# Performance work log

Hardware: AMD Instinct MI355X
Metric: run time of the kernel (lower is better)

Reference implementation:

```python
import jax, jax.numpy as jnp
import numpy as np
import math

B, C, D, NH, L, DFF = 128, 112, 512, 8, 13, 1920
DK = D // NH  # 64
_pos = np.arange(64)
_ranks, _files = _pos // 8, _pos % 8
RIDX = np.clip(_ranks[:, None] - _ranks[None, :], -7, 7) + 7  # [64,64] rel-rank bucket
FIDX = np.clip(_files[:, None] - _files[None, :], -7, 7) + 7  # [64,64] rel-file bucket
DIAG = _ranks + _files        # [64] in [0,14]
ADIAG = _ranks - _files + 7   # [64] in [0,14]


def _ln(x, g, b):
    m = jnp.mean(x, -1, keepdims=True)
    v = jnp.mean((x - m) ** 2, -1, keepdims=True)
    return (x - m) * jax.lax.rsqrt(v + 1e-5) * g + b


def setup_inputs() -> dict:
    key = jax.random.key(0)
    ks = iter(jax.random.split(key, 40))
    nrm = lambda *s: jax.random.normal(next(ks), s, jnp.float32) * 0.02
    return dict(
        x=jax.random.normal(next(ks), (B, C, 8, 8), jnp.float32),
        conv_w=nrm(C, D), conv_b=jnp.zeros(D),
        cls_token=nrm(1, 1, D),
        abs_pos=nrm(1, 64, D),
        file_emb=nrm(8, D), rank_emb=nrm(8, D),
        diag_emb=nrm(15, D), anti_diag_emb=nrm(15, D),
        ln1_g=jnp.ones((L, D)), ln1_b=jnp.zeros((L, D)),
        wq=nrm(L, D, D), bq=jnp.zeros((L, D)),
        wk=nrm(L, D, D), bk=jnp.zeros((L, D)),
        wv=nrm(L, D, D), bv=jnp.zeros((L, D)),
        wo=nrm(L, D, D), bo=jnp.zeros((L, D)),
        rel_bias=nrm(L, 15, 15, NH),
        ln2_g=jnp.ones((L, D)), ln2_b=jnp.zeros((L, D)),
        w_ff1=nrm(L, D, 2 * DFF), b_ff1=jnp.zeros((L, 2 * DFF)),
        w_ff2=nrm(L, DFF, D), b_ff2=jnp.zeros((L, D)),
        out_g=jnp.ones(D), out_b=jnp.zeros(D),
        vw1=nrm(D, D // 2), vb1=jnp.zeros(D // 2),
        vw2=nrm(D // 2, 128), vb2=jnp.zeros(128),
        vw3=nrm(128, 3), vb3=jnp.zeros(3),
        pw=nrm(D, 72), pb=jnp.zeros(72),
    )


def reference(x, conv_w, conv_b, cls_token, abs_pos, file_emb, rank_emb, diag_emb, anti_diag_emb,
              ln1_g, ln1_b, wq, bq, wk, bk, wv, bv, wo, bo, rel_bias, ln2_g, ln2_b,
              w_ff1, b_ff1, w_ff2, b_ff2, out_g, out_b,
              vw1, vb1, vw2, vb2, vw3, vb3, pw, pb):
    Bc = x.shape[0]
    # 1x1 conv == channel-wise linear; flatten spatial (row-major: s = rank*8 + file)
    tok = jnp.einsum('bcs,cd->bsd', x.reshape(Bc, C, 64), conv_w) + conv_b  # [B,64,D]
    pos = abs_pos + file_emb[_files] + rank_emb[_ranks] + diag_emb[DIAG] + anti_diag_emb[ADIAG]
    tok = tok + pos
    h = jnp.concatenate([jnp.broadcast_to(cls_token, (Bc, 1, D)), tok], axis=1)  # [B,65,D]
    scale = 1.0 / math.sqrt(DK)

    def block(hx, p):
        g1, b1, Wq, Bq, Wk, Bk, Wv, Bv, Wo, Bo, rb, g2, b2, W1, B1, W2, B2 = p
        n = _ln(hx, g1, b1)
        q = (n @ Wq + Bq).reshape(Bc, 65, NH, DK).transpose(0, 2, 1, 3)
        k = (n @ Wk + Bk).reshape(Bc, 65, NH, DK).transpose(0, 2, 1, 3)
        v = (n @ Wv + Bv).reshape(Bc, 65, NH, DK).transpose(0, 2, 1, 3)
        # gather relative-position bias [64,64,H] -> [H,65,65] with zero row/col for CLS
        bias = jnp.pad(jnp.transpose(rb[RIDX, FIDX], (2, 0, 1)), ((0, 0), (1, 0), (1, 0)))
        scores = jnp.einsum('bhqd,bhkd->bhqk', q, k) * scale + bias[None]
        a = jax.nn.softmax(scores, axis=-1)
        ctx = jnp.einsum('bhqk,bhkd->bhqd', a, v).transpose(0, 2, 1, 3).reshape(Bc, 65, D)
        hx = hx + ctx @ Wo + Bo
        n2 = _ln(hx, g2, b2)
        u = n2 @ W1 + B1
        u1, u2 = jnp.split(u, 2, axis=-1)
        hx = hx + (jax.nn.gelu(u1, approximate=False) * u2) @ W2 + B2
        return hx, None

    params = (ln1_g, ln1_b, wq, bq, wk, bk, wv, bv, wo, bo, rel_bias,
              ln2_g, ln2_b, w_ff1, b_ff1, w_ff2, b_ff2)
    h, _ = jax.lax.scan(block, h, params)
    h = _ln(h, out_g, out_b)
    cls = h[:, 0]
    v1 = jax.nn.gelu(cls @ vw1 + vb1, approximate=False)
    v2 = jax.nn.gelu(v1 @ vw2 + vb2, approximate=False)
    value = v2 @ vw3 + vb3                 # WDL logits [B,3]
    policy = (h[:, 1:] @ pw + pb).reshape(Bc, -1)  # [B, 64*72]
    return policy, value
```

## Files before the change

kernel.cpp:

```cpp
#include <hip/hip_runtime.h>
#include <stdint.h>

#define NLAYER 13
#define DMODEL 512
#define SEQ    65
#define BATCH  128
#define MROWS  (BATCH*SEQ)
#define NHEAD  8
#define DFFH   1920
#define MTILES 65
#define MBAND  9

typedef __bf16 bf16x8 __attribute__((ext_vector_type(8)));
typedef float  f32x4  __attribute__((ext_vector_type(4)));

__device__ __forceinline__ float bf2f(unsigned short u) {
    union { unsigned int i; float f; } c; c.i = ((unsigned int)u) << 16; return c.f;
}
__device__ __forceinline__ unsigned short f2bf(float f) {
    union { float f; unsigned int i; } c; c.f = f;
    unsigned int u = c.i;
    u += 0x7fffu + ((u >> 16) & 1u);
    return (unsigned short)(u >> 16);
}
__device__ __forceinline__ float gelu_exact(float x) {
    return 0.5f * x * (1.0f + erff(x * 0.70710678118654752f));
}

__global__ __launch_bounds__(256) void transpose_f32_bf16(
    const float* __restrict__ src, unsigned short* __restrict__ dst,
    int R, int C, int Cpad, long srcLS, long dstLS, int rowOff)
{
    __shared__ float tile[32][33];
    int l  = blockIdx.z;
    int c0 = blockIdx.x * 32, r0 = blockIdx.y * 32;
    const float* s = src + (long)l * srcLS;
    unsigned short* d = dst + (long)l * dstLS;
    int tx = threadIdx.x, ty = threadIdx.y;
#pragma unroll
    for (int k = 0; k < 4; k++) {
        int r = r0 + ty + 8*k, c = c0 + tx;
        float v = (r < R && c < C) ? s[(long)r * C + c] : 0.0f;
        tile[ty + 8*k][tx] = v;
    }
    __syncthreads();
#pragma unroll
    for (int k = 0; k < 4; k++) {
        int c = c0 + ty + 8*k, r = r0 + tx;
        if (c < Cpad && r < R)
            d[(long)(rowOff + c) * R + r] = f2bf(tile[tx][ty + 8*k]);
    }
}

__global__ __launch_bounds__(256) void stack_bias_kernel(
    const float* __restrict__ bq, const float* __restrict__ bk,
    const float* __restrict__ bv, float* __restrict__ bqkv)
{
    int idx = blockIdx.x * 256 + threadIdx.x;
    if (idx >= NLAYER * 1536) return;
    int l = idx / 1536, r = idx - l * 1536;
    float v;
    if (r < 512)       v = bq[l*512 + r];
    else if (r < 1024) v = bk[l*512 + r - 512];
    else               v = bv[l*512 + r - 1024];
    bqkv[idx] = v;
}

__global__ __launch_bounds__(256) void embed_kernel(
    const float* __restrict__ x, const float* __restrict__ conv_w,
    const float* __restrict__ conv_b, const float* __restrict__ cls_tok,
    const float* __restrict__ abs_pos, const float* __restrict__ file_emb,
    const float* __restrict__ rank_emb, const float* __restrict__ diag_emb,
    const float* __restrict__ adiag_emb, float* __restrict__ h)
{
    int b = blockIdx.y, sg = blockIdx.x, t = threadIdx.x;
    if (sg == 8) {
        for (int d = t; d < 512; d += 256)
            h[(long)b * SEQ * 512 + d] = cls_tok[d];
        return;
    }
    __shared__ float xs[112][8];
    for (int idx = t; idx < 112*8; idx += 256) {
        int c = idx >> 3, j = idx & 7;
        xs[c][j] = x[((long)b*112 + c)*64 + sg*8 + j];
    }
    __syncthreads();
    int d0 = t, d1 = t + 256;
    float acc0[8] = {}, acc1[8] = {};
    for (int c = 0; c < 112; c++) {
        float w0 = conv_w[c*512 + d0], w1 = conv_w[c*512 + d1];
#pragma unroll
        for (int j = 0; j < 8; j++) { acc0[j] += xs[c][j]*w0; acc1[j] += xs[c][j]*w1; }
    }
#pragma unroll
    for (int j = 0; j < 8; j++) {
        int sq = sg*8 + j, r = sq >> 3, f = sq & 7;
        long row = ((long)b * SEQ + 1 + sq) * 512;
        h[row + d0] = acc0[j] + conv_b[d0] + abs_pos[sq*512+d0] + file_emb[f*512+d0]
                    + rank_emb[r*512+d0] + diag_emb[(r+f)*512+d0] + adiag_emb[(r-f+7)*512+d0];
        h[row + d1] = acc1[j] + conv_b[d1] + abs_pos[sq*512+d1] + file_emb[f*512+d1]
                    + rank_emb[r*512+d1] + diag_emb[(r+f)*512+d1] + adiag_emb[(r-f+7)*512+d1];
    }
}

__global__ __launch_bounds__(256) void ln_kernel(
    const float* __restrict__ hx, const float* __restrict__ g,
    const float* __restrict__ bb, unsigned short* __restrict__ o)
{
    int row  = blockIdx.x * 4 + (threadIdx.x >> 6);
    int lane = threadIdx.x & 63;
    const float4* xr = (const float4*)(hx + (long)row * 512);
    float4 v0 = xr[lane], v1 = xr[lane + 64];
    float s  = v0.x+v0.y+v0.z+v0.w + v1.x+v1.y+v1.z+v1.w;
    float s2 = v0.x*v0.x+v0.y*v0.y+v0.z*v0.z+v0.w*v0.w
             + v1.x*v1.x+v1.y*v1.y+v1.z*v1.z+v1.w*v1.w;
    for (int off = 32; off; off >>= 1) { s += __shfl_xor(s, off); s2 += __shfl_xor(s2, off); }
    float mean = s * (1.0f/512.0f);
    float var  = s2 * (1.0f/512.0f) - mean*mean;
    float rs   = rsqrtf(var + 1e-5f);
    const float4* gr = (const float4*)g; const float4* br = (const float4*)bb;
    float4 g0 = gr[lane], g1 = gr[lane+64], b0 = br[lane], b1 = br[lane+64];
    ushort4 o0, o1;
    o0.x = f2bf((v0.x-mean)*rs*g0.x + b0.x);
    o0.y = f2bf((v0.y-mean)*rs*g0.y + b0.y);
    o0.z = f2bf((v0.z-mean)*rs*g0.z + b0.z);
    o0.w = f2bf((v0.w-mean)*rs*g0.w + b0.w);
    o1.x = f2bf((v1.x-mean)*rs*g1.x + b1.x);
    o1.y = f2bf((v1.y-mean)*rs*g1.y + b1.y);
    o1.z = f2bf((v1.z-mean)*rs*g1.z + b1.z);
    o1.w = f2bf((v1.w-mean)*rs*g1.w + b1.w);
    ushort4* orow = (ushort4*)(o + (long)row * 512);
    orow[lane] = o0; orow[lane + 64] = o1;
}

template<int MODE>
__global__ __launch_bounds__(256) void gemm128(
    const unsigned short* __restrict__ A, const unsigned short* __restrict__ Bt,
    const float* __restrict__ bias, const float* __restrict__ res,
    void* __restrict__ out, int K, int ldo, int nT)
{
    __shared__ __attribute__((aligned(16))) unsigned short As[2*128*32];
    __shared__ __attribute__((aligned(16))) unsigned short Bs[2*128*32];
    int id = blockIdx.x;
    int xcd = id & 7, jj = id >> 3;
    int bn  = jj % nT;
    int mt  = xcd * MBAND + jj / nT;
    if (mt >= MTILES) return;
    int m0 = mt * 128;
    int tid = threadIdx.x;
    int lane = tid & 63, w = tid >> 6;
    int quad = lane >> 4, col = lane & 15;

    int srow = tid >> 2;
    int sc8  = (tid & 3) * 8;

    int br0, br1;
    if (MODE == 2) {
        br0 = bn*64 + srow;
        br1 = 1920 + bn*64 + srow;
    } else {
        br0 = bn*128 + srow;
        br1 = bn*128 + srow + 64;
    }
    const unsigned short* Arow0 = A + (long)(m0 + srow) * K + sc8;
    const unsigned short* Arow1 = A + (long)(m0 + srow + 64) * K + sc8;
    const unsigned short* Brow0 = Bt + (long)br0 * K + sc8;
    const unsigned short* Brow1 = Bt + (long)br1 * K + sc8;

    f32x4 acc[2][8] = {};

    int4 ca0 = *(const int4*)(Arow0);
    int4 ca1 = *(const int4*)(Arow1);
    int4 cb0 = *(const int4*)(Brow0);
    int4 cb1 = *(const int4*)(Brow1);
    *(int4*)(&As[srow*32 + sc8])        = ca0;
    *(int4*)(&As[(srow+64)*32 + sc8])   = ca1;
    *(int4*)(&Bs[srow*32 + sc8])        = cb0;
    *(int4*)(&Bs[(srow+64)*32 + sc8])   = cb1;
    ca0 = *(const int4*)(Arow0 + 32);
    ca1 = *(const int4*)(Arow1 + 32);
    cb0 = *(const int4*)(Brow0 + 32);
    cb1 = *(const int4*)(Brow1 + 32);
    __syncthreads();

#define GSTEP(BUFC, BUFN, kt)                                                  \
    {                                                                          \
        bf16x8 af[2], bfr[8];                                                  \
        _Pragma("unroll")                                                      \
        for (int i = 0; i < 2; i++)                                            \
            af[i] = *(const bf16x8*)(&As[(BUFC) + (w*32 + i*16 + col)*32 + quad*8]); \
        _Pragma("unroll")                                                      \
        for (int t = 0; t < 8; t++)                                            \
            bfr[t] = *(const bf16x8*)(&Bs[(BUFC) + (t*16 + col)*32 + quad*8]); \
        if ((kt) + 32 < K) {                                                   \
            *(int4*)(&As[(BUFN) + srow*32 + sc8])      = ca0;                  \
            *(int4*)(&As[(BUFN) + (srow+64)*32 + sc8]) = ca1;                  \
            *(int4*)(&Bs[(BUFN) + srow*32 + sc8])      = cb0;                  \
            *(int4*)(&Bs[(BUFN) + (srow+64)*32 + sc8]) = cb1;                  \
            if ((kt) + 64 < K) {                                               \
                ca0 = *(const int4*)(Arow0 + (kt) + 64);                       \
                ca1 = *(const int4*)(Arow1 + (kt) + 64);                       \
                cb0 = *(const int4*)(Brow0 + (kt) + 64);                       \
                cb1 = *(const int4*)(Brow1 + (kt) + 64);                       \
            }                                                                  \
        }                                                                      \
        _Pragma("unroll")                                                      \
        for (int i = 0; i < 2; i++)                                            \
        _Pragma("unroll")                                                      \
            for (int t = 0; t < 8; t++)                                        \
                acc[i][t] = __builtin_amdgcn_mfma_f32_16x16x32_bf16(af[i], bfr[t], acc[i][t], 0, 0, 0); \
        __syncthreads();                                                       \
    }

    for (int k0 = 0; k0 < K; k0 += 64) {
        GSTEP(0,    4096, k0);
        GSTEP(4096, 0,    k0 + 32);
    }
#undef GSTEP

    if (MODE == 2) {
        unsigned short* O = (unsigned short*)out;
        int gn0 = bn * 64;
#pragma unroll
        for (int i = 0; i < 2; i++)
#pragma unroll
        for (int t = 0; t < 4; t++) {
            int c = t*16 + col;
            float b1v = bias[gn0 + c];
            float b2v = bias[1920 + gn0 + c];
#pragma unroll
            for (int r = 0; r < 4; r++) {
                int m = m0 + w*32 + i*16 + quad*4 + r;
                float u1 = acc[i][t][r]   + b1v;
                float u2 = acc[i][t+4][r] + b2v;
                O[(long)m * DFFH + gn0 + c] = f2bf(gelu_exact(u1) * u2);
            }
        }
        return;
    }
    int n0 = bn * 128;
#pragma unroll
    for (int i = 0; i < 2; i++)
#pragma unroll
    for (int t = 0; t < 8; t++) {
        int cg = n0 + t*16 + col;
        float bv = (MODE == 3) ? (cg < 72 ? bias[cg] : 0.0f) : bias[cg];
#pragma unroll
        for (int r = 0; r < 4; r++) {
            int m = m0 + w*32 + i*16 + quad*4 + r;
            float v = acc[i][t][r] + bv;
            if (MODE == 0) {
                ((unsigned short*)out)[(long)m * ldo + cg] = f2bf(v);
            } else if (MODE == 1) {
                ((float*)out)[(long)m * ldo + cg] = res[(long)m * ldo + cg] + v;
            } else {
                if (cg < 72) {
                    int b2 = m / 65, s = m - b2 * 65;
                    if (s > 0)
                        ((float*)out)[(long)b2 * 4608 + (s - 1) * 72 + cg] = v;
                }
            }
        }
    }
}

__global__ __launch_bounds__(256) void attn_mfma_kernel(
    const unsigned short* __restrict__ qkv,
    const float* __restrict__ rel_bias,
    unsigned short* __restrict__ ctx,
    int layer)
{
    constexpr int QS = 72;
    constexpr int VS = 104;
    constexpr int SS = 68;
    constexpr int PS = 104;
    __shared__ __attribute__((aligned(16))) unsigned short Qs[80*QS];
    __shared__ __attribute__((aligned(16))) unsigned short Ks[80*QS];
    __shared__ __attribute__((aligned(16))) unsigned short Vt[64*VS];
    __shared__ __attribute__((aligned(16))) float Sf[65*SS];
    __shared__ __attribute__((aligned(16))) unsigned short Pb[80*PS];
    __shared__ float bias_s[225];

    int h = blockIdx.x, b = blockIdx.y, t = threadIdx.x;
    int lane = t & 63, w = t >> 6;
    int quad = lane >> 4, col = lane & 15;

    for (int i = t; i < 225; i += 256)
        bias_s[i] = rel_bias[((long)layer*225 + i)*8 + h];

    for (int i = t; i < 65*8; i += 256) {
        int s = i >> 3, c8 = (i & 7) * 8;
        const unsigned short* row = qkv + ((long)(b*65+s))*1536 + h*64 + c8;
        int4 qv = *(const int4*)(row);
        int4 kv = *(const int4*)(row + 512);
        int4 vv = *(const int4*)(row + 1024);
        unsigned short qsc[8];
        const unsigned short* qp = (const unsigned short*)&qv;
#pragma unroll
        for (int j = 0; j < 8; j++) qsc[j] = f2bf(bf2f(qp[j]) * 0.125f);
        *(int4*)&Qs[s*QS + c8] = *(const int4*)qsc;
        *(int4*)&Ks[s*QS + c8] = kv;
        const unsigned short* vp = (const unsigned short*)&vv;
#pragma unroll
        for (int j = 0; j < 8; j++) Vt[(c8+j)*VS + s] = vp[j];
    }
    for (int i = t; i < 64*31; i += 256) {
        int d = i / 31, s = 65 + i % 31;
        Vt[d*VS + s] = 0;
    }
    __syncthreads();

    for (int tt = w; tt < 25; tt += 4) {
        int mi = tt / 5, nj = tt % 5;
        f32x4 acc = {};
        bf16x8 a0 = *(const bf16x8*)&Qs[(mi*16+col)*QS + quad*8];
        bf16x8 b0 = *(const bf16x8*)&Ks[(nj*16+col)*QS + quad*8];
        acc = __builtin_amdgcn_mfma_f32_16x16x32_bf16(a0, b0, acc, 0, 0, 0);
        bf16x8 a1 = *(const bf16x8*)&Qs[(mi*16+col)*QS + 32 + quad*8];
        bf16x8 b1 = *(const bf16x8*)&Ks[(nj*16+col)*QS + 32 + quad*8];
        acc = __builtin_amdgcn_mfma_f32_16x16x32_bf16(a1, b1, acc, 0, 0, 0);
#pragma unroll
        for (int r = 0; r < 4; r++) {
            int qi = mi*16 + quad*4 + r, kj = nj*16 + col;
            if (qi < 65 && kj < 65) {
                float v = acc[r];
                if (qi >= 1 && kj >= 1) {
                    int i2 = qi - 1, j2 = kj - 1;
                    int dr = (i2 >> 3) - (j2 >> 3) + 7;
                    int df = (i2 & 7) - (j2 & 7) + 7;
                    v += bias_s[dr*15 + df];
                }
                Sf[qi*SS + kj] = v;
            }
        }
    }
    __syncthreads();

    for (int r = w; r < 65; r += 4) {
        float x0 = Sf[r*SS + lane];
        float x1 = (lane == 0) ? Sf[r*SS + 64] : -1e30f;
        float mx = fmaxf(x0, x1);
        for (int off = 32; off; off >>= 1) mx = fmaxf(mx, __shfl_xor(mx, off));
        float e0 = __expf(x0 - mx);
        float e1 = (lane == 0) ? __expf(x1 - mx) : 0.0f;
        float sm = e0 + e1;
        for (int off = 32; off; off >>= 1) sm += __shfl_xor(sm, off);
        float inv = 1.0f / sm;
        Pb[r*PS + lane] = f2bf(e0 * inv);
        if (lane == 0)  Pb[r*PS + 64] = f2bf(e1 * inv);
        if (lane >= 1 && lane <= 31) Pb[r*PS + 64 + lane] = 0;
    }
    __syncthreads();

    for (int tt = w; tt < 20; tt += 4) {
        int mi = tt >> 2, dj = tt & 3;
        f32x4 acc = {};
#pragma unroll
        for (int ks = 0; ks < 3; ks++) {
            bf16x8 a  = *(const bf16x8*)&Pb[(mi*16+col)*PS + ks*32 + quad*8];
            bf16x8 bb = *(const bf16x8*)&Vt[(dj*16+col)*VS + ks*32 + quad*8];
            acc = __builtin_amdgcn_mfma_f32_16x16x32_bf16(a, bb, acc, 0, 0, 0);
        }
#pragma unroll
        for (int r = 0; r < 4; r++) {
            int qi = mi*16 + quad*4 + r;
            if (qi < 65)
                ctx[((long)(b*65+qi))*512 + h*64 + dj*16 + col] = f2bf(acc[r]);
        }
    }
}

__global__ __launch_bounds__(256) void value_head_kernel(
    const unsigned short* __restrict__ hn,
    const float* __restrict__ vw1, const float* __restrict__ vb1,
    const float* __restrict__ vw2, const float* __restrict__ vb2,
    const float* __restrict__ vw3, const float* __restrict__ vb3,
    float* __restrict__ outv)
{
    int b = blockIdx.x, t = threadIdx.x;
    __shared__ float cls[512], v1[256], v2[128];
    for (int d = t; d < 512; d += 256) cls[d] = bf2f(hn[(long)b * SEQ * 512 + d]);
    __syncthreads();
    {
        float a = vb1[t];
        for (int c = 0; c < 512; c++) a += cls[c] * vw1[c*256 + t];
        v1[t] = gelu_exact(a);
    }
    __syncthreads();
    if (t < 128) {
        float a = vb2[t];
        for (int c = 0; c < 256; c++) a += v1[c] * vw2[c*128 + t];
        v2[t] = gelu_exact(a);
    }
    __syncthreads();
    if (t < 3) {
        float a = vb3[t];
        for (int c = 0; c < 128; c++) a += v2[c] * vw3[c*3 + t];
        outv[b*3 + t] = a;
    }
}

extern "C" void kernel_launch(void* const* d_in, const int* in_sizes, int n_in,
                              void* d_out, int out_size, void* d_ws, size_t ws_size,
                              hipStream_t stream)
{
    (void)in_sizes; (void)n_in; (void)out_size; (void)ws_size;
    const float* x        = (const float*)d_in[0];
    const float* conv_w   = (const float*)d_in[1];
    const float* conv_b   = (const float*)d_in[2];
    const float* cls_tok  = (const float*)d_in[3];
    const float* abs_pos  = (const float*)d_in[4];
    const float* file_emb = (const float*)d_in[5];
    const float* rank_emb = (const float*)d_in[6];
    const float* diag_emb = (const float*)d_in[7];
    const float* adiag    = (const float*)d_in[8];
    const float* ln1_g    = (const float*)d_in[9];
    const float* ln1_b    = (const float*)d_in[10];
    const float* wq       = (const float*)d_in[11];
    const float* bq       = (const float*)d_in[12];
    const float* wk       = (const float*)d_in[13];
    const float* bk       = (const float*)d_in[14];
    const float* wv       = (const float*)d_in[15];
    const float* bv       = (const float*)d_in[16];
    const float* wo       = (const float*)d_in[17];
    const float* bo       = (const float*)d_in[18];
    const float* rel_bias = (const float*)d_in[19];
    const float* ln2_g    = (const float*)d_in[20];
    const float* ln2_b    = (const float*)d_in[21];
    const float* w_ff1    = (const float*)d_in[22];
    const float* b_ff1    = (const float*)d_in[23];
    const float* w_ff2    = (const float*)d_in[24];
    const float* b_ff2    = (const float*)d_in[25];
    const float* out_g    = (const float*)d_in[26];
    const float* out_b    = (const float*)d_in[27];
    const float* vw1      = (const float*)d_in[28];
    const float* vb1      = (const float*)d_in[29];
    const float* vw2      = (const float*)d_in[30];
    const float* vb2      = (const float*)d_in[31];
    const float* vw3      = (const float*)d_in[32];
    const float* vb3      = (const float*)d_in[33];
    const float* pw       = (const float*)d_in[34];
    const float* pb       = (const float*)d_in[35];

    char* p = (char*)d_ws;
    auto alloc = [&](size_t bytes) { void* r = (void*)p; p += (bytes + 255) & ~(size_t)255; return r; };
    unsigned short* qkvT = (unsigned short*)alloc((size_t)NLAYER*1536*512*2);
    unsigned short* woT  = (unsigned short*)alloc((size_t)NLAYER*512*512*2);
    unsigned short* w1T  = (unsigned short*)alloc((size_t)NLAYER*3840*512*2);
    unsigned short* w2T  = (unsigned short*)alloc((size_t)NLAYER*512*1920*2);
    unsigned short* pwT  = (unsigned short*)alloc((size_t)128*512*2);
    float*          bqkv = (float*)alloc((size_t)NLAYER*1536*4);
    float*          h    = (float*)alloc((size_t)MROWS*512*4);
    unsigned short* nbf  = (unsigned short*)alloc((size_t)MROWS*512*2);
    unsigned short* qkvb = (unsigned short*)alloc((size_t)MROWS*1536*2);
    unsigned short* ctxb = (unsigned short*)alloc((size_t)MROWS*512*2);
    unsigned short* gbuf = (unsigned short*)alloc((size_t)MROWS*1920*2);

    dim3 tb(32, 8);
    transpose_f32_bf16<<<dim3(16,16,NLAYER), tb, 0, stream>>>(wq, qkvT, 512, 512, 512, 512L*512, 1536L*512, 0);
    transpose_f32_bf16<<<dim3(16,16,NLAYER), tb, 0, stream>>>(wk, qkvT, 512, 512, 512, 512L*512, 1536L*512, 512);
    transpose_f32_bf16<<<dim3(16,16,NLAYER), tb, 0, stream>>>(wv, qkvT, 512, 512, 512, 512L*512, 1536L*512, 1024);
    transpose_f32_bf16<<<dim3(16,16,NLAYER), tb, 0, stream>>>(wo, woT, 512, 512, 512, 512L*512, 512L*512, 0);
    transpose_f32_bf16<<<dim3(120,16,NLAYER), tb, 0, stream>>>(w_ff1, w1T, 512, 3840, 3840, 512L*3840, 3840L*512, 0);
    transpose_f32_bf16<<<dim3(16,60,NLAYER), tb, 0, stream>>>(w_ff2, w2T, 1920, 512, 512, 1920L*512, 512L*1920, 0);
    transpose_f32_bf16<<<dim3(4,16,1), tb, 0, stream>>>(pw, pwT, 512, 72, 128, 0, 0, 0);
    stack_bias_kernel<<<(NLAYER*1536 + 255)/256, 256, 0, stream>>>(bq, bk, bv, bqkv);

    embed_kernel<<<dim3(9, BATCH), 256, 0, stream>>>(x, conv_w, conv_b, cls_tok, abs_pos,
                                                     file_emb, rank_emb, diag_emb, adiag, h);

    for (int l = 0; l < NLAYER; l++) {
        ln_kernel<<<MROWS/4, 256, 0, stream>>>(h, ln1_g + l*512, ln1_b + l*512, nbf);
        gemm128<0><<<72*12, 256, 0, stream>>>(nbf, qkvT + (size_t)l*1536*512,
                                              bqkv + l*1536, nullptr, qkvb, 512, 1536, 12);
        attn_mfma_kernel<<<dim3(NHEAD, BATCH), 256, 0, stream>>>(qkvb, rel_bias, ctxb, l);
        gemm128<1><<<72*4, 256, 0, stream>>>(ctxb, woT + (size_t)l*512*512,
                                             bo + l*512, h, h, 512, 512, 4);
        ln_kernel<<<MROWS/4, 256, 0, stream>>>(h, ln2_g + l*512, ln2_b + l*512, nbf);
        gemm128<2><<<72*30, 256, 0, stream>>>(nbf, w1T + (size_t)l*3840*512,
                                              b_ff1 + l*3840, nullptr, gbuf, 512, 0, 30);
        gemm128<1><<<72*4, 256, 0, stream>>>(gbuf, w2T + (size_t)l*512*1920,
                                             b_ff2 + l*512, h, h, 1920, 512, 4);
    }

    ln_kernel<<<MROWS/4, 256, 0, stream>>>(h, out_g, out_b, nbf);
    gemm128<3><<<72*1, 256, 0, stream>>>(nbf, pwT, pb, nullptr, (float*)d_out, 512, 0, 1);
    value_head_kernel<<<BATCH, 256, 0, stream>>>(nbf, vw1, vb1, vw2, vb2, vw3, vb3,
                                                 (float*)d_out + (size_t)BATCH*4608);
}
```

Before: 2.833 ms.

## Use 2x2 wave tiling and XOR-swizzled LDS layout in GEMM kernel

Changes the 128x128 GEMM warp layout from 4x1 (each wave 32 rows by 128 cols) to 2x2 (each wave 64x64), so each wave does 8 LDS fragment reads per k-step instead of 10. It also XOR-swizzles the 16-byte column chunks in shared memory by row to reduce LDS bank conflicts on fragment reads. For the gated FFN mode, the B rows are reordered so each column-wave holds matching gate and value halves. This adds index arithmetic and remaps the epilogue.

```diff
diff --git a/kernel.cpp b/kernel.cpp
--- a/kernel.cpp
+++ b/kernel.cpp
@@ -149,15 +149,17 @@
     int m0 = mt * 128;
     int tid = threadIdx.x;
     int lane = tid & 63, w = tid >> 6;
+    int wr = w >> 1, wc = w & 1;
     int quad = lane >> 4, col = lane & 15;
 
     int srow = tid >> 2;
     int sc8  = (tid & 3) * 8;
+    int scS  = sc8 ^ ((srow & 3) * 8);
 
     int br0, br1;
     if (MODE == 2) {
-        br0 = bn*64 + srow;
-        br1 = 1920 + bn*64 + srow;
+        br0 = ((srow >> 5) & 1) * 1920 + bn*64 + (srow & 31);
+        br1 = ((srow >> 5) & 1) * 1920 + bn*64 + 32 + (srow & 31);
     } else {
         br0 = bn*128 + srow;
         br1 = bn*128 + srow + 64;
@@ -167,16 +169,17 @@
     const unsigned short* Brow0 = Bt + (long)br0 * K + sc8;
     const unsigned short* Brow1 = Bt + (long)br1 * K + sc8;
 
-    f32x4 acc[2][8] = {};
+    f32x4 acc[4][4] = {};
+    int rk = (quad * 8) ^ ((col & 3) * 8);
 
     int4 ca0 = *(const int4*)(Arow0);
     int4 ca1 = *(const int4*)(Arow1);
     int4 cb0 = *(const int4*)(Brow0);
     int4 cb1 = *(const int4*)(Brow1);
-    *(int4*)(&As[srow*32 + sc8])        = ca0;
-    *(int4*)(&As[(srow+64)*32 + sc8])   = ca1;
-    *(int4*)(&Bs[srow*32 + sc8])        = cb0;
-    *(int4*)(&Bs[(srow+64)*32 + sc8])   = cb1;
+    *(int4*)(&As[srow*32 + scS])        = ca0;
+    *(int4*)(&As[(srow+64)*32 + scS])   = ca1;
+    *(int4*)(&Bs[srow*32 + scS])        = cb0;
+    *(int4*)(&Bs[(srow+64)*32 + scS])   = cb1;
     ca0 = *(const int4*)(Arow0 + 32);
     ca1 = *(const int4*)(Arow1 + 32);
     cb0 = *(const int4*)(Brow0 + 32);
@@ -185,18 +188,18 @@
 
 #define GSTEP(BUFC, BUFN, kt)                                                  \
     {                                                                          \
-        bf16x8 af[2], bfr[8];                                                  \
+        bf16x8 af[4], bfr[4];                                                  \
         _Pragma("unroll")                                                      \
-        for (int i = 0; i < 2; i++)                                            \
-            af[i] = *(const bf16x8*)(&As[(BUFC) + (w*32 + i*16 + col)*32 + quad*8]); \
+        for (int i = 0; i < 4; i++)                                            \
+            af[i] = *(const bf16x8*)(&As[(BUFC) + (wr*64 + i*16 + col)*32 + rk]); \
         _Pragma("unroll")                                                      \
-        for (int t = 0; t < 8; t++)                                            \
-            bfr[t] = *(const bf16x8*)(&Bs[(BUFC) + (t*16 + col)*32 + quad*8]); \
+        for (int j = 0; j < 4; j++)                                            \
+            bfr[j] = *(const bf16x8*)(&Bs[(BUFC) + (wc*64 + j*16 + col)*32 + rk]); \
         if ((kt) + 32 < K) {                                                   \
-            *(int4*)(&As[(BUFN) + srow*32 + sc8])      = ca0;                  \
-            *(int4*)(&As[(BUFN) + (srow+64)*32 + sc8]) = ca1;                  \
-            *(int4*)(&Bs[(BUFN) + srow*32 + sc8])      = cb0;                  \
-            *(int4*)(&Bs[(BUFN) + (srow+64)*32 + sc8]) = cb1;                  \
+            *(int4*)(&As[(BUFN) + srow*32 + scS])      = ca0;                  \
+            *(int4*)(&As[(BUFN) + (srow+64)*32 + scS]) = ca1;                  \
+            *(int4*)(&Bs[(BUFN) + srow*32 + scS])      = cb0;                  \
+            *(int4*)(&Bs[(BUFN) + (srow+64)*32 + scS]) = cb1;                  \
             if ((kt) + 64 < K) {                                               \
                 ca0 = *(const int4*)(Arow0 + (kt) + 64);                       \
                 ca1 = *(const int4*)(Arow1 + (kt) + 64);                       \
@@ -205,10 +208,10 @@
             }                                                                  \
         }                                                                      \
         _Pragma("unroll")                                                      \
-        for (int i = 0; i < 2; i++)                                            \
+        for (int i = 0; i < 4; i++)                                            \
         _Pragma("unroll")                                                      \
-            for (int t = 0; t < 8; t++)                                        \
-                acc[i][t] = __builtin_amdgcn_mfma_f32_16x16x32_bf16(af[i], bfr[t], acc[i][t], 0, 0, 0); \
+            for (int j = 0; j < 4; j++)                                        \
+                acc[i][j] = __builtin_amdgcn_mfma_f32_16x16x32_bf16(af[i], bfr[j], acc[i][j], 0, 0, 0); \
         __syncthreads();                                                       \
     }
 
@@ -222,17 +225,17 @@
         unsigned short* O = (unsigned short*)out;
         int gn0 = bn * 64;
 #pragma unroll
-        for (int i = 0; i < 2; i++)
-#pragma unroll
-        for (int t = 0; t < 4; t++) {
-            int c = t*16 + col;
+        for (int i = 0; i < 4; i++)
+#pragma unroll
+        for (int j = 0; j < 2; j++) {
+            int c = wc*32 + j*16 + col;
             float b1v = bias[gn0 + c];
             float b2v = bias[1920 + gn0 + c];
 #pragma unroll
             for (int r = 0; r < 4; r++) {
-                int m = m0 + w*32 + i*16 + quad*4 + r;
-                float u1 = acc[i][t][r]   + b1v;
-                float u2 = acc[i][t+4][r] + b2v;
+                int m = m0 + wr*64 + i*16 + quad*4 + r;
+                float u1 = acc[i][j][r]   + b1v;
+                float u2 = acc[i][j+2][r] + b2v;
                 O[(long)m * DFFH + gn0 + c] = f2bf(gelu_exact(u1) * u2);
             }
         }
@@ -240,15 +243,15 @@
     }
     int n0 = bn * 128;
 #pragma unroll
-    for (int i = 0; i < 2; i++)
-#pragma unroll
-    for (int t = 0; t < 8; t++) {
-        int cg = n0 + t*16 + col;
+    for (int i = 0; i < 4; i++)
+#pragma unroll
+    for (int j = 0; j < 4; j++) {
+        int cg = n0 + wc*64 + j*16 + col;
         float bv = (MODE == 3) ? (cg < 72 ? bias[cg] : 0.0f) : bias[cg];
 #pragma unroll
         for (int r = 0; r < 4; r++) {
-            int m = m0 + w*32 + i*16 + quad*4 + r;
-            float v = acc[i][t][r] + bv;
+            int m = m0 + wr*64 + i*16 + quad*4 + r;
+            float v = acc[i][j][r] + bv;
             if (MODE == 0) {
                 ((unsigned short*)out)[(long)m * ldo + cg] = f2bf(v);
             } else if (MODE == 1) {
```

Measured after the change: 2.783 ms. About the same (-1.7%).
